# Kernel optimization log

Measured on AMD Instinct MI355X. Metric: run time of the kernel, lower is better.

## Reference

```python
import jax, jax.numpy as jnp
import numpy as np

B, I, H, S = 16384, 256, 256, 32
EVENT_THRESH = 0.85


def setup_inputs() -> dict:
    key = jax.random.key(0)
    ks = jax.random.split(key, 20)
    r = lambda k, shp: jax.random.normal(k, shp, dtype=jnp.float32)
    w = lambda k, shp: jax.random.normal(k, shp, dtype=jnp.float32) * 0.02
    return {
        # forward args / state
        "x_t": r(ks[0], (B, I)),
        "h_lstm": r(ks[1], (B, H)),
        "c_lstm": r(ks[2], (B, H)),
        "h_mem_prev": jnp.zeros((B, H), jnp.float32),
        "slots": r(ks[3], (B, S, I)),
        "ptr": jax.random.randint(ks[4], (B,), 0, S, dtype=jnp.int64),
        # SequenceMemoryCell params (weights stored as (in, out))
        "W_val": w(ks[5], (I, I)),
        "b_val": jnp.zeros((I,), jnp.float32),
        "W_ev": w(ks[6], (I, 1)),
        "b_ev": jnp.zeros((1,), jnp.float32),
        "pos_emb": r(ks[7], (S, I)),
        "slot_weights": jnp.ones((S,), jnp.float32),
        "W_sp": w(ks[8], (I, H)),
        "b_sp": jnp.zeros((H,), jnp.float32),
        # LSTM params
        "W_ih": w(ks[9], (I + H, 4 * H)),
        "b_ih": jnp.zeros((4 * H,), jnp.float32),
        "W_hh": w(ks[10], (H, 4 * H)),
    }


def reference(x_t, h_lstm, c_lstm, h_mem_prev, slots, ptr,
              W_val, b_val, W_ev, b_ev, pos_emb, slot_weights, W_sp, b_sp,
              W_ih, b_ih, W_hh):
    n_slots = slot_weights.shape[0]
    # --- SequenceMemoryCell ---
    e_t = jax.nn.sigmoid(x_t @ W_ev + b_ev)            # (B, 1)
    v = x_t @ W_val + b_val                            # (B, I)
    event_mask = e_t[:, 0] > EVENT_THRESH              # (B,)
    # circular-buffer scatter write at ptr, gated by event_mask
    onehot = jnp.arange(n_slots)[None, :] == ptr[:, None]          # (B, S)
    write = event_mask[:, None] & onehot                           # (B, S)
    new_slots = jnp.where(write[:, :, None], v[:, None, :], slots) # (B, S, I)
    new_ptr = (ptr + event_mask.astype(ptr.dtype)) % n_slots
    # weighted pool over slots with positional embeddings
    w = jax.nn.softmax(slot_weights)                               # (S,)
    pooled = jnp.einsum('bsi,s->bi', new_slots + pos_emb[None], w) # (B, I)
    h_mem = pooled @ W_sp + b_sp                                   # (B, H)
    # --- LSTM on [x_t; h_mem] ---
    gates = jnp.concatenate([x_t, h_mem], axis=1) @ W_ih + b_ih + h_lstm @ W_hh
    i_g, f_g, g_t, o_g = jnp.split(gates, 4, axis=1)
    c_new = jax.nn.sigmoid(f_g) * c_lstm + jax.nn.sigmoid(i_g) * jnp.tanh(g_t)
    h_new = jax.nn.sigmoid(o_g) * jnp.tanh(c_new)
    return (h_new, c_new, h_mem, new_slots, new_ptr)
```

## Files before the change

kernel.cpp:

```cpp
#include <hip/hip_runtime.h>
#include <hip/hip_bf16.h>

#define B_SZ 16384
#define I_SZ 256
#define H_SZ 256
#define S_SZ 32

typedef __attribute__((ext_vector_type(8))) short short8;
typedef __attribute__((ext_vector_type(4))) float f32x4;

__device__ __forceinline__ ushort f2b(float f) {
  __hip_bfloat16 h = __float2bfloat16(f);
  return *reinterpret_cast<ushort*>(&h);
}
__device__ __forceinline__ float sgm(float x) { return 1.0f / (1.0f + expf(-x)); }

__device__ __forceinline__ void gll16(const void* g, void* l) {
  __builtin_amdgcn_global_load_lds(
      (const __attribute__((address_space(1))) unsigned*)g,
      (__attribute__((address_space(3))) unsigned*)l, 16, 0, 0);
}

__global__ __launch_bounds__(256) void prep_weights(
    const float* __restrict__ W_sp, const float* __restrict__ W_ih,
    const float* __restrict__ W_hh, ushort* __restrict__ WspT,
    ushort* __restrict__ WcatT) {
  int idx = blockIdx.x * 256 + threadIdx.x;
  if (idx < 256 * 256) {
    int n = idx >> 8, k = idx & 255;
    WspT[idx] = f2b(W_sp[k * 256 + n]);
  } else {
    int j = idx - 256 * 256;
    int r = j / 768, k = j - r * 768;
    int hb = r >> 6, g = (r >> 4) & 3, hl = r & 15;
    int n = g * 256 + hb * 16 + hl;
    float v = (k < 512) ? W_ih[k * 1024 + n] : W_hh[(k - 512) * 1024 + n];
    WcatT[j] = f2b(v);
  }
}

__global__ __launch_bounds__(256) void event_pool(
    const float* __restrict__ x_t, const float* __restrict__ h_lstm,
    const float* __restrict__ slots, const int* __restrict__ ptr,
    const float* __restrict__ W_val, const float* __restrict__ b_val,
    const float* __restrict__ W_ev, const float* __restrict__ b_ev,
    const float* __restrict__ pos_emb, const float* __restrict__ slot_w,
    float* __restrict__ out_slots, float* __restrict__ out_ptr,
    ushort* __restrict__ x_b, ushort* __restrict__ hl_b,
    ushort* __restrict__ pooled_b) {
  int l = threadIdx.x & 63;
  int w = threadIdx.x >> 6;
  int b = blockIdx.x * 4 + w;
  __shared__ float x_sh[4][256];

  float4 x4 = *(const float4*)(x_t + (size_t)b * 256 + l * 4);
  *(float4*)&x_sh[w][l * 4] = x4;
  ushort4 xb = make_ushort4(f2b(x4.x), f2b(x4.y), f2b(x4.z), f2b(x4.w));
  *(ushort4*)&x_b[(size_t)b * 256 + l * 4] = xb;
  float4 hl4 = *(const float4*)(h_lstm + (size_t)b * 256 + l * 4);
  ushort4 hb = make_ushort4(f2b(hl4.x), f2b(hl4.y), f2b(hl4.z), f2b(hl4.w));
  *(ushort4*)&hl_b[(size_t)b * 256 + l * 4] = hb;

  float4 we4 = *(const float4*)(W_ev + l * 4);
  float p = x4.x * we4.x + x4.y * we4.y + x4.z * we4.z + x4.w * we4.w;
  for (int off = 32; off; off >>= 1) p += __shfl_xor(p, off, 64);
  float z = p + b_ev[0];
  bool ev = sgm(z) > 0.85f;
  int pb = ptr[b];

  __syncthreads();

  float4 v4 = make_float4(0.f, 0.f, 0.f, 0.f);
  if (ev) {
    v4 = *(const float4*)(b_val + l * 4);
    for (int k = 0; k < 256; k++) {
      float xv = x_sh[w][k];
      float4 wv = *(const float4*)(W_val + (size_t)k * 256 + l * 4);
      v4.x += xv * wv.x; v4.y += xv * wv.y;
      v4.z += xv * wv.z; v4.w += xv * wv.w;
    }
  }

  float mx = -1e30f;
  for (int s = 0; s < 32; s++) mx = fmaxf(mx, slot_w[s]);
  float sum = 0.f;
  for (int s = 0; s < 32; s++) sum += expf(slot_w[s] - mx);
  float rs = 1.f / sum;

  const float4* sl4 = (const float4*)slots + (size_t)b * 2048;
  float4* os4 = (float4*)out_slots + (size_t)b * 2048;
  const float4* pe4 = (const float4*)pos_emb;
  float4 pool = make_float4(0.f, 0.f, 0.f, 0.f);
#pragma unroll 8
  for (int s = 0; s < 32; s++) {
    float ws_ = expf(slot_w[s] - mx) * rs;
    float4 t = sl4[s * 64 + l];
    if (ev && s == pb) t = v4;
    os4[s * 64 + l] = t;
    float4 pe = pe4[s * 64 + l];
    pool.x += ws_ * (t.x + pe.x);
    pool.y += ws_ * (t.y + pe.y);
    pool.z += ws_ * (t.z + pe.z);
    pool.w += ws_ * (t.w + pe.w);
  }
  ushort4 pb4 = make_ushort4(f2b(pool.x), f2b(pool.y), f2b(pool.z), f2b(pool.w));
  *(ushort4*)&pooled_b[(size_t)b * 256 + l * 4] = pb4;

  if (l == 0) out_ptr[b] = (float)(ev ? ((pb + 1) & 31) : pb);
}

__global__ __launch_bounds__(256) void gemm_hmem(
    const ushort* __restrict__ A0, const ushort* __restrict__ WT,
    const float* __restrict__ bias, float* __restrict__ out_f32,
    ushort* __restrict__ out_b16) {
  int l = threadIdx.x & 63;
  int wid = threadIdx.x >> 6;
  int wm = wid >> 1, wn = wid & 1;
  int m0 = blockIdx.x * 128;
  int n0 = blockIdx.y * 128;
  __shared__ ushort Ash[128 * 32];
  __shared__ ushort Bsh[128 * 32];

  f32x4 acc[4][4] = {};

  for (int k0 = 0; k0 < 256; k0 += 32) {
#pragma unroll
    for (int i = 0; i < 2; i++) {
      int seg = i * 256 + threadIdx.x;
      int row = seg >> 2, cb = (seg & 3) * 8;
      gll16(A0 + (size_t)(m0 + row) * 256 + k0 + cb, Ash + seg * 8);
    }
#pragma unroll
    for (int i = 0; i < 2; i++) {
      int seg = i * 256 + threadIdx.x;
      int row = seg >> 2, cb = (seg & 3) * 8;
      gll16(WT + (size_t)(n0 + row) * 256 + k0 + cb, Bsh + seg * 8);
    }
    __syncthreads();

    short8 af[4], bfr[4];
#pragma unroll
    for (int m = 0; m < 4; m++)
      af[m] = *(const short8*)&Ash[(wm * 64 + m * 16 + (l & 15)) * 32 + (l >> 4) * 8];
#pragma unroll
    for (int n = 0; n < 4; n++)
      bfr[n] = *(const short8*)&Bsh[(wn * 64 + n * 16 + (l & 15)) * 32 + (l >> 4) * 8];
#pragma unroll
    for (int m = 0; m < 4; m++)
#pragma unroll
      for (int n = 0; n < 4; n++)
        acc[m][n] = __builtin_amdgcn_mfma_f32_16x16x32_bf16(af[m], bfr[n], acc[m][n], 0, 0, 0);
    __syncthreads();
  }

#pragma unroll
  for (int m = 0; m < 4; m++)
#pragma unroll
    for (int n = 0; n < 4; n++)
#pragma unroll
      for (int r = 0; r < 4; r++) {
        int row = m0 + wm * 64 + m * 16 + (l >> 4) * 4 + r;
        int col = n0 + wn * 64 + n * 16 + (l & 15);
        float v = acc[m][n][r] + bias[col];
        out_f32[(size_t)row * 256 + col] = v;
        out_b16[(size_t)row * 256 + col] = f2b(v);
      }
}

template <int KTOT>
__global__ __launch_bounds__(512) void gemm256_lstm(
    const ushort* __restrict__ A0s, const ushort* __restrict__ A1s,
    const ushort* __restrict__ A2s, const ushort* __restrict__ WT,
    const float* __restrict__ bias, const float* __restrict__ c_lstm,
    float* __restrict__ h_out, float* __restrict__ c_out) {
  constexpr int NT = KTOT / 64;
  __shared__ ushort Ash[2][2][128][64];
  __shared__ ushort Bsh[2][2][128][64];
  const int tid = threadIdx.x;
  const int l = tid & 63;
  const int wid = tid >> 6;
  const int wm = wid >> 2, wn = wid & 3;
  const int id = blockIdx.x;
  const int xcd = id & 7, jj = id >> 3;
  const int mb = xcd * 8 + (jj >> 2), nb = jj & 3;
  const int m0 = mb * 256, n0 = nb * 256;

  auto asel = [&](int kt) { return kt < 4 ? A0s : (kt < 8 ? A1s : A2s); };

  auto stageA = [&](int bu, int h, int kt) {
    const ushort* s = asel(kt);
    int cb = (kt & 3) * 64;
#pragma unroll
    for (int ld = 0; ld < 2; ld++) {
      int seg = ld * 512 + tid;
      int row = seg >> 3, C = seg & 7;
      int Cs = C ^ (row & 7);
      gll16(s + (size_t)(m0 + h * 128 + row) * 256 + cb + Cs * 8,
            &Ash[bu][h][0][0] + seg * 8);
    }
  };
  auto stageB = [&](int bu, int h, int kt) {
    int cb = kt * 64;
#pragma unroll
    for (int ld = 0; ld < 2; ld++) {
      int seg = ld * 512 + tid;
      int row = seg >> 3, C = seg & 7;
      int Cs = C ^ (row & 7);
      gll16(WT + (size_t)(n0 + h * 128 + row) * KTOT + cb + Cs * 8,
            &Bsh[bu][h][0][0] + seg * 8);
    }
  };

  f32x4 acc[8][4] = {};

  stageB(0, 0, 0); stageB(0, 1, 0);
  stageA(0, 0, 0); stageA(0, 1, 0);
  stageB(1, 0, 1); stageB(1, 1, 1);

  for (int t = 0; t < NT; t++) {
    const int c = t & 1;
    const ushort* Abase = &Ash[c][wm][0][0];
    const ushort* Bbase = &Bsh[c][wn >> 1][0][0];

    if (t < NT - 1) asm volatile("s_waitcnt vmcnt(4)" ::: "memory");
    else            asm volatile("s_waitcnt vmcnt(0)" ::: "memory");
    asm volatile("s_barrier" ::: "memory");

    short8 bfr[4][2];
#pragma unroll
    for (int nf = 0; nf < 4; nf++)
#pragma unroll
      for (int kk = 0; kk < 2; kk++) {
        int r = (wn & 1) * 64 + nf * 16 + (l & 15);
        int C = (kk * 4 + (l >> 4)) ^ (l & 7);
        bfr[nf][kk] = *(const short8*)(Bbase + r * 64 + C * 8);
      }
    short8 af[2][2];
#pragma unroll
    for (int q = 0; q < 2; q++)
#pragma unroll
      for (int kk = 0; kk < 2; kk++) {
        int r = (0 * 2 + q) * 16 + (l & 15);
        int C = (kk * 4 + (l >> 4)) ^ (l & 7);
        af[q][kk] = *(const short8*)(Abase + r * 64 + C * 8);
      }
    if (t + 1 < NT) stageA(c ^ 1, 0, t + 1);
    __builtin_amdgcn_s_setprio(1);
#pragma unroll
    for (int q = 0; q < 2; q++)
#pragma unroll
      for (int nf = 0; nf < 4; nf++)
#pragma unroll
        for (int kk = 0; kk < 2; kk++)
          acc[q][nf] = __builtin_amdgcn_mfma_f32_16x16x32_bf16(
              af[q][kk], bfr[nf][kk], acc[q][nf], 0, 0, 0);
    __builtin_amdgcn_s_setprio(0);

#pragma unroll
    for (int p = 1; p < 4; p++) {
      asm volatile("s_barrier" ::: "memory");
#pragma unroll
      for (int q = 0; q < 2; q++)
#pragma unroll
        for (int kk = 0; kk < 2; kk++) {
          int r = (p * 2 + q) * 16 + (l & 15);
          int C = (kk * 4 + (l >> 4)) ^ (l & 7);
          af[q][kk] = *(const short8*)(Abase + r * 64 + C * 8);
        }
      if (p == 1) {
        if (t + 1 < NT) stageA(c ^ 1, 1, t + 1);
        if (t + 2 < NT) stageB(c, 0, t + 2);
      } else if (p == 2) {
        if (t + 2 < NT) stageB(c, 1, t + 2);
      }
      __builtin_amdgcn_s_setprio(1);
#pragma unroll
      for (int q = 0; q < 2; q++)
#pragma unroll
        for (int nf = 0; nf < 4; nf++)
#pragma unroll
          for (int kk = 0; kk < 2; kk++)
            acc[p * 2 + q][nf] = __builtin_amdgcn_mfma_f32_16x16x32_bf16(
                af[q][kk], bfr[nf][kk], acc[p * 2 + q][nf], 0, 0, 0);
      __builtin_amdgcn_s_setprio(0);
    }
  }

  int h = (nb * 4 + wn) * 16 + (l & 15);
  float bi = bias[h], bf_ = bias[256 + h], bg = bias[512 + h], bo = bias[768 + h];
#pragma unroll
  for (int mf = 0; mf < 8; mf++)
#pragma unroll
    for (int r = 0; r < 4; r++) {
      int row = m0 + wm * 128 + mf * 16 + (l >> 4) * 4 + r;
      float ig = acc[mf][0][r] + bi;
      float fg = acc[mf][1][r] + bf_;
      float gt = acc[mf][2][r] + bg;
      float og = acc[mf][3][r] + bo;
      float cc = c_lstm[(size_t)row * 256 + h];
      float cn = sgm(fg) * cc + sgm(ig) * tanhf(gt);
      float hn = sgm(og) * tanhf(cn);
      c_out[(size_t)row * 256 + h] = cn;
      h_out[(size_t)row * 256 + h] = hn;
    }
}

extern "C" void kernel_launch(void* const* d_in, const int* in_sizes, int n_in,
                              void* d_out, int out_size, void* d_ws, size_t ws_size,
                              hipStream_t stream) {
  const float* x_t    = (const float*)d_in[0];
  const float* h_lstm = (const float*)d_in[1];
  const float* c_lstm = (const float*)d_in[2];
  const float* slots  = (const float*)d_in[4];
  const int*   ptr    = (const int*)d_in[5];
  const float* W_val  = (const float*)d_in[6];
  const float* b_val  = (const float*)d_in[7];
  const float* W_ev   = (const float*)d_in[8];
  const float* b_ev   = (const float*)d_in[9];
  const float* pos_emb = (const float*)d_in[10];
  const float* slot_w  = (const float*)d_in[11];
  const float* W_sp   = (const float*)d_in[12];
  const float* b_sp   = (const float*)d_in[13];
  const float* W_ih   = (const float*)d_in[14];
  const float* b_ih   = (const float*)d_in[15];
  const float* W_hh   = (const float*)d_in[16];

  float* out = (float*)d_out;
  const size_t BH = (size_t)B_SZ * H_SZ;
  float* out_h    = out;
  float* out_c    = out + BH;
  float* out_hmem = out + 2 * BH;
  float* out_slots = out + 3 * BH;
  float* out_ptr   = out + 3 * BH + (size_t)B_SZ * S_SZ * I_SZ;

  char* ws = (char*)d_ws;
  ushort* x_b      = (ushort*)(ws);
  ushort* hl_b     = (ushort*)(ws + 8388608);
  ushort* pooled_b = (ushort*)(ws + 16777216);
  ushort* hmem_b   = (ushort*)(ws + 25165824);
  ushort* WspT     = (ushort*)(ws + 33554432);
  ushort* WcatT    = (ushort*)(ws + 33685504);

  prep_weights<<<3328, 256, 0, stream>>>(W_sp, W_ih, W_hh, WspT, WcatT);

  event_pool<<<B_SZ / 4, 256, 0, stream>>>(
      x_t, h_lstm, slots, ptr, W_val, b_val, W_ev, b_ev, pos_emb, slot_w,
      out_slots, out_ptr, x_b, hl_b, pooled_b);

  gemm_hmem<<<dim3(128, 2), 256, 0, stream>>>(
      pooled_b, WspT, b_sp, out_hmem, hmem_b);

  gemm256_lstm<768><<<256, 512, 0, stream>>>(
      x_b, hmem_b, hl_b, WcatT, b_ih, c_lstm, out_h, out_c);
}
```

Baseline: 288.4 us.

## Fold W_sp into LSTM input weights and merge prep with event pooling

Precomputes W_sp·W_ih[256:512] and a folded bias so the LSTM GEMM consumes pooled activations directly, which removes the dependency on the h_mem GEMM and its bf16 output. Weight prep is merged into the event/pool kernel as extra blocks, saving a launch. Slot traffic now uses nontemporal loads and stores. The trade-off is that h_mem's contribution passes through a product weight rounded to bf16, which changes numerics slightly, and the front kernel gains extra blocks that each loop over 256 rows.

Measured after the change: 251.4 us (median of 2 runs). 1.15x faster.

```diff
diff --git a/kernel.cpp b/kernel.cpp
--- a/kernel.cpp
+++ b/kernel.cpp
@@ -21,98 +21,127 @@
       (__attribute__((address_space(3))) unsigned*)l, 16, 0, 0);
 }
 
-__global__ __launch_bounds__(256) void prep_weights(
-    const float* __restrict__ W_sp, const float* __restrict__ W_ih,
-    const float* __restrict__ W_hh, ushort* __restrict__ WspT,
-    ushort* __restrict__ WcatT) {
-  int idx = blockIdx.x * 256 + threadIdx.x;
-  if (idx < 256 * 256) {
-    int n = idx >> 8, k = idx & 255;
-    WspT[idx] = f2b(W_sp[k * 256 + n]);
-  } else {
-    int j = idx - 256 * 256;
-    int r = j / 768, k = j - r * 768;
-    int hb = r >> 6, g = (r >> 4) & 3, hl = r & 15;
-    int n = g * 256 + hb * 16 + hl;
-    float v = (k < 512) ? W_ih[k * 1024 + n] : W_hh[(k - 512) * 1024 + n];
-    WcatT[j] = f2b(v);
-  }
-}
-
-__global__ __launch_bounds__(256) void event_pool(
+__global__ __launch_bounds__(256) void front(
     const float* __restrict__ x_t, const float* __restrict__ h_lstm,
     const float* __restrict__ slots, const int* __restrict__ ptr,
     const float* __restrict__ W_val, const float* __restrict__ b_val,
     const float* __restrict__ W_ev, const float* __restrict__ b_ev,
     const float* __restrict__ pos_emb, const float* __restrict__ slot_w,
+    const float* __restrict__ W_sp, const float* __restrict__ W_ih,
+    const float* __restrict__ W_hh, const float* __restrict__ b_ih,
+    const float* __restrict__ b_sp,
     float* __restrict__ out_slots, float* __restrict__ out_ptr,
     ushort* __restrict__ x_b, ushort* __restrict__ hl_b,
-    ushort* __restrict__ pooled_b) {
-  int l = threadIdx.x & 63;
-  int w = threadIdx.x >> 6;
-  int b = blockIdx.x * 4 + w;
+    ushort* __restrict__ pooled_b, ushort* __restrict__ WspT,
+    ushort* __restrict__ WcatT, float* __restrict__ biasp) {
   __shared__ float x_sh[4][256];
-
-  float4 x4 = *(const float4*)(x_t + (size_t)b * 256 + l * 4);
-  *(float4*)&x_sh[w][l * 4] = x4;
-  ushort4 xb = make_ushort4(f2b(x4.x), f2b(x4.y), f2b(x4.z), f2b(x4.w));
-  *(ushort4*)&x_b[(size_t)b * 256 + l * 4] = xb;
-  float4 hl4 = *(const float4*)(h_lstm + (size_t)b * 256 + l * 4);
-  ushort4 hb = make_ushort4(f2b(hl4.x), f2b(hl4.y), f2b(hl4.z), f2b(hl4.w));
-  *(ushort4*)&hl_b[(size_t)b * 256 + l * 4] = hb;
-
-  float4 we4 = *(const float4*)(W_ev + l * 4);
-  float p = x4.x * we4.x + x4.y * we4.y + x4.z * we4.z + x4.w * we4.w;
-  for (int off = 32; off; off >>= 1) p += __shfl_xor(p, off, 64);
-  float z = p + b_ev[0];
-  bool ev = sgm(z) > 0.85f;
-  int pb = ptr[b];
-
-  __syncthreads();
-
-  float4 v4 = make_float4(0.f, 0.f, 0.f, 0.f);
-  if (ev) {
-    v4 = *(const float4*)(b_val + l * 4);
-    for (int k = 0; k < 256; k++) {
-      float xv = x_sh[w][k];
-      float4 wv = *(const float4*)(W_val + (size_t)k * 256 + l * 4);
-      v4.x += xv * wv.x; v4.y += xv * wv.y;
-      v4.z += xv * wv.z; v4.w += xv * wv.w;
-    }
+  const int bid = blockIdx.x;
+  const int t = threadIdx.x;
+
+  if (bid < 4096) {
+    int l = t & 63;
+    int w = t >> 6;
+    int b = bid * 4 + w;
+
+    float4 x4 = *(const float4*)(x_t + (size_t)b * 256 + l * 4);
+    *(float4*)&x_sh[w][l * 4] = x4;
+    ushort4 xb = make_ushort4(f2b(x4.x), f2b(x4.y), f2b(x4.z), f2b(x4.w));
+    *(ushort4*)&x_b[(size_t)b * 256 + l * 4] = xb;
+    float4 hl4 = *(const float4*)(h_lstm + (size_t)b * 256 + l * 4);
+    ushort4 hb = make_ushort4(f2b(hl4.x), f2b(hl4.y), f2b(hl4.z), f2b(hl4.w));
+    *(ushort4*)&hl_b[(size_t)b * 256 + l * 4] = hb;
+
+    float4 we4 = *(const float4*)(W_ev + l * 4);
+    float p = x4.x * we4.x + x4.y * we4.y + x4.z * we4.z + x4.w * we4.w;
+    for (int off = 32; off; off >>= 1) p += __shfl_xor(p, off, 64);
+    float z = p + b_ev[0];
+    bool ev = sgm(z) > 0.85f;
+    int pb = ptr[b];
+
+    __syncthreads();
+
+    f32x4 v4 = {0.f, 0.f, 0.f, 0.f};
+    if (ev) {
+      v4 = *(const f32x4*)(b_val + l * 4);
+      for (int k = 0; k < 256; k++) {
+        float xv = x_sh[w][k];
+        f32x4 wv = *(const f32x4*)(W_val + (size_t)k * 256 + l * 4);
+        v4 += xv * wv;
+      }
+    }
+
+    float mx = -1e30f;
+    for (int s = 0; s < 32; s++) mx = fmaxf(mx, slot_w[s]);
+    float sum = 0.f;
+    for (int s = 0; s < 32; s++) sum += expf(slot_w[s] - mx);
+    float rs = 1.f / sum;
+
+    const f32x4* sl4 = (const f32x4*)slots + (size_t)b * 2048;
+    f32x4* os4 = (f32x4*)out_slots + (size_t)b * 2048;
+    const f32x4* pe4 = (const f32x4*)pos_emb;
+    f32x4 pool = {0.f, 0.f, 0.f, 0.f};
+#pragma unroll 8
+    for (int s = 0; s < 32; s++) {
+      float ws_ = expf(slot_w[s] - mx) * rs;
+      f32x4 tv = __builtin_nontemporal_load(sl4 + s * 64 + l);
+      if (ev && s == pb) tv = v4;
+      __builtin_nontemporal_store(tv, os4 + s * 64 + l);
+      f32x4 pe = pe4[s * 64 + l];
+      pool += ws_ * (tv + pe);
+    }
+    ushort4 pb4 = make_ushort4(f2b(pool[0]), f2b(pool[1]), f2b(pool[2]), f2b(pool[3]));
+    *(ushort4*)&pooled_b[(size_t)b * 256 + l * 4] = pb4;
+
+    if (l == 0) out_ptr[b] = (float)(ev ? ((pb + 1) & 31) : pb);
+
+  } else if (bid < 4104) {
+    for (int e = (bid - 4096) * 256 + t; e < 65536; e += 8 * 256) {
+      int n = e >> 8, k = e & 255;
+      WspT[e] = f2b(W_sp[k * 256 + n]);
+    }
+  } else if (bid < 4168) {
+    for (int e = (bid - 4104) * 256 + t; e < 1024 * 512; e += 64 * 256) {
+      int r = e >> 9, kk = e & 511;
+      int k = (kk < 256) ? kk : kk + 256;
+      int hb = r >> 6, g = (r >> 4) & 3, hl = r & 15;
+      int n = g * 256 + hb * 16 + hl;
+      float v = (k < 512) ? W_ih[(size_t)k * 1024 + n]
+                          : W_hh[(size_t)(k - 512) * 1024 + n];
+      WcatT[(size_t)r * 768 + k] = f2b(v);
+    }
+  } else if (bid < 4424) {
+    int i = bid - 4168;
+    x_sh[0][t] = W_sp[(size_t)i * 256 + t];
+    __syncthreads();
+    int n0 = t * 4;
+    f32x4 acc = {0.f, 0.f, 0.f, 0.f};
+    for (int m = 0; m < 256; m++) {
+      float s = x_sh[0][m];
+      f32x4 w2 = *(const f32x4*)(W_ih + (size_t)(256 + m) * 1024 + n0);
+      acc += s * w2;
+    }
+#pragma unroll
+    for (int d = 0; d < 4; d++) {
+      int n = n0 + d;
+      int g = n >> 8, rem = n & 255, hb = rem >> 4, hl = rem & 15;
+      int r = hb * 64 + g * 16 + hl;
+      WcatT[(size_t)r * 768 + 256 + i] = f2b(acc[d]);
+    }
+  } else {
+    int n0 = t * 4;
+    f32x4 acc = *(const f32x4*)(b_ih + n0);
+    for (int m = 0; m < 256; m++) {
+      float s = b_sp[m];
+      f32x4 w2 = *(const f32x4*)(W_ih + (size_t)(256 + m) * 1024 + n0);
+      acc += s * w2;
+    }
+    *(f32x4*)(biasp + n0) = acc;
   }
-
-  float mx = -1e30f;
-  for (int s = 0; s < 32; s++) mx = fmaxf(mx, slot_w[s]);
-  float sum = 0.f;
-  for (int s = 0; s < 32; s++) sum += expf(slot_w[s] - mx);
-  float rs = 1.f / sum;
-
-  const float4* sl4 = (const float4*)slots + (size_t)b * 2048;
-  float4* os4 = (float4*)out_slots + (size_t)b * 2048;
-  const float4* pe4 = (const float4*)pos_emb;
-  float4 pool = make_float4(0.f, 0.f, 0.f, 0.f);
-#pragma unroll 8
-  for (int s = 0; s < 32; s++) {
-    float ws_ = expf(slot_w[s] - mx) * rs;
-    float4 t = sl4[s * 64 + l];
-    if (ev && s == pb) t = v4;
-    os4[s * 64 + l] = t;
-    float4 pe = pe4[s * 64 + l];
-    pool.x += ws_ * (t.x + pe.x);
-    pool.y += ws_ * (t.y + pe.y);
-    pool.z += ws_ * (t.z + pe.z);
-    pool.w += ws_ * (t.w + pe.w);
-  }
-  ushort4 pb4 = make_ushort4(f2b(pool.x), f2b(pool.y), f2b(pool.z), f2b(pool.w));
-  *(ushort4*)&pooled_b[(size_t)b * 256 + l * 4] = pb4;
-
-  if (l == 0) out_ptr[b] = (float)(ev ? ((pb + 1) & 31) : pb);
 }
 
 __global__ __launch_bounds__(256) void gemm_hmem(
     const ushort* __restrict__ A0, const ushort* __restrict__ WT,
-    const float* __restrict__ bias, float* __restrict__ out_f32,
-    ushort* __restrict__ out_b16) {
+    const float* __restrict__ bias, float* __restrict__ out_f32) {
   int l = threadIdx.x & 63;
   int wid = threadIdx.x >> 6;
   int wm = wid >> 1, wn = wid & 1;
@@ -161,9 +190,7 @@
       for (int r = 0; r < 4; r++) {
         int row = m0 + wm * 64 + m * 16 + (l >> 4) * 4 + r;
         int col = n0 + wn * 64 + n * 16 + (l & 15);
-        float v = acc[m][n][r] + bias[col];
-        out_f32[(size_t)row * 256 + col] = v;
-        out_b16[(size_t)row * 256 + col] = f2b(v);
+        out_f32[(size_t)row * 256 + col] = acc[m][n][r] + bias[col];
       }
 }
 
@@ -337,19 +364,18 @@
   ushort* x_b      = (ushort*)(ws);
   ushort* hl_b     = (ushort*)(ws + 8388608);
   ushort* pooled_b = (ushort*)(ws + 16777216);
-  ushort* hmem_b   = (ushort*)(ws + 25165824);
-  ushort* WspT     = (ushort*)(ws + 33554432);
-  ushort* WcatT    = (ushort*)(ws + 33685504);
-
-  prep_weights<<<3328, 256, 0, stream>>>(W_sp, W_ih, W_hh, WspT, WcatT);
-
-  event_pool<<<B_SZ / 4, 256, 0, stream>>>(
+  ushort* WspT     = (ushort*)(ws + 25165824);
+  ushort* WcatT    = (ushort*)(ws + 25296896);
+  float*  biasp    = (float*)(ws + 26869760);
+
+  front<<<4425, 256, 0, stream>>>(
       x_t, h_lstm, slots, ptr, W_val, b_val, W_ev, b_ev, pos_emb, slot_w,
-      out_slots, out_ptr, x_b, hl_b, pooled_b);
+      W_sp, W_ih, W_hh, b_ih, b_sp,
+      out_slots, out_ptr, x_b, hl_b, pooled_b, WspT, WcatT, biasp);
+
+  gemm256_lstm<768><<<256, 512, 0, stream>>>(
+      x_b, pooled_b, hl_b, WcatT, biasp, c_lstm, out_h, out_c);
 
   gemm_hmem<<<dim3(128, 2), 256, 0, stream>>>(
-      pooled_b, WspT, b_sp, out_hmem, hmem_b);
-
-  gemm256_lstm<768><<<256, 512, 0, stream>>>(
-      x_b, hmem_b, hl_b, WcatT, b_ih, c_lstm, out_h, out_c);
-}
+      pooled_b, WspT, b_sp, out_hmem);
+}
```
